# Kernel optimization log

Measured on AMD Instinct MI355X. Metric: run time of the kernel, lower is better.

## Reference

```python
import jax, jax.numpy as jnp
import numpy as np

EMBED = 2048
HEADS = 16
DFF = 4 * EMBED
EPS = 1e-5


def layernorm(x, g, b):
    mu = jnp.mean(x, axis=-1, keepdims=True)
    var = jnp.var(x, axis=-1, keepdims=True)
    return (x - mu) * jax.lax.rsqrt(var + EPS) * g + b


def setup_inputs() -> dict:
    key = jax.random.key(0)
    ks = jax.random.split(key, 16)
    s = 1.0 / np.sqrt(EMBED)
    sf = 1.0 / np.sqrt(DFF)
    return {
        "x": jax.random.normal(ks[0], (2, 2048, EMBED), jnp.float32),
        "Wq": jax.random.normal(ks[1], (EMBED, EMBED), jnp.float32) * s,
        "bq": jnp.zeros((EMBED,), jnp.float32),
        "Wk": jax.random.normal(ks[2], (EMBED, EMBED), jnp.float32) * s,
        "bk": jnp.zeros((EMBED,), jnp.float32),
        "Wv": jax.random.normal(ks[3], (EMBED, EMBED), jnp.float32) * s,
        "bv": jnp.zeros((EMBED,), jnp.float32),
        "Wo": jax.random.normal(ks[4], (EMBED, EMBED), jnp.float32) * s,
        "bo": jnp.zeros((EMBED,), jnp.float32),
        "g1": jnp.ones((EMBED,), jnp.float32),
        "b1": jnp.zeros((EMBED,), jnp.float32),
        "g2": jnp.ones((EMBED,), jnp.float32),
        "b2": jnp.zeros((EMBED,), jnp.float32),
        "W1": jax.random.normal(ks[5], (EMBED, DFF), jnp.float32) * s,
        "bf1": jnp.zeros((DFF,), jnp.float32),
        "W2": jax.random.normal(ks[6], (DFF, EMBED), jnp.float32) * sf,
        "bf2": jnp.zeros((EMBED,), jnp.float32),
    }


def reference(x, Wq, bq, Wk, bk, Wv, bv, Wo, bo, g1, b1, g2, b2, W1, bf1, W2, bf2):
    B, N, C = x.shape
    H = HEADS
    hd = C // H
    # QKV projections -> [B, H, N, hd]
    def split_heads(t):
        return t.reshape(B, N, H, hd).transpose(0, 2, 1, 3)
    q = split_heads(x @ Wq + bq)
    k = split_heads(x @ Wk + bk)
    v = split_heads(x @ Wv + bv)
    # scores [B, H, N, N]
    attn = jnp.einsum('bhqd,bhkd->bhqk', q, k) / np.sqrt(hd)
    attn = jax.nn.softmax(attn, axis=-1)
    out = jnp.einsum('bhqk,bhkd->bhqd', attn, v)
    out = out.transpose(0, 2, 1, 3).reshape(B, N, C)
    out = out @ Wo + bo
    h = layernorm(x + out, g1, b1)
    ff = jax.nn.gelu(h @ W1 + bf1, approximate=False) @ W2 + bf2
    return layernorm(h + ff, g2, b2)
```

## Files before the change

kernel.cpp:

```cpp
#include <hip/hip_runtime.h>
#include <math.h>

#define EMBED 2048
#define DFF   8192
#define TOK   4096
#define SEQ   2048
#define HEADS 16
#define HD    128
#define LDQ   6144

typedef __attribute__((ext_vector_type(8))) short short8;
typedef __attribute__((ext_vector_type(4))) float f32x4;

__device__ __forceinline__ unsigned short f2bf(float f) {
    unsigned int u = __float_as_uint(f);
    return (unsigned short)((u + 0x7FFFu + ((u >> 16) & 1u)) >> 16);
}
__device__ __forceinline__ float bf2f(unsigned short s) {
    return __uint_as_float(((unsigned int)s) << 16);
}

__device__ __forceinline__ void async16(const void* g, void* l) {
    __builtin_amdgcn_global_load_lds((const __attribute__((address_space(1))) void*)g,
                                     (__attribute__((address_space(3))) void*)l, 16, 0, 0);
}

__device__ __forceinline__ float gelu_fast(float v) {
    const float y = 1.5957691216057308f * (v + 0.044715f * v * v * v);
    return v / (1.0f + __expf(-y));
}

template<int MODE>
__global__ __launch_bounds__(256, 2)
void gemm_bf16(const unsigned short* __restrict__ A, const unsigned short* __restrict__ B,
               const float* __restrict__ bias, const void* __restrict__ resid,
               unsigned short* __restrict__ C, int M, int N, int K, int lda)
{
    __shared__ __align__(16) float smemf[8448];
    unsigned short* As = (unsigned short*)smemf;
    unsigned short* Bs = As + 8192;
    float* Cs = smemf;

    const int t = threadIdx.x;
    const int w = t >> 6, l = t & 63;
    const int quad = l >> 4, m16 = l & 15;
    const long bm = (long)blockIdx.y * 128, bn = (long)blockIdx.x * 128;
    const int wr = (w >> 1)*64, wc = (w & 1)*64;

    f32x4 acc[4][4] = {};

    const int srow = w*16 + (l >> 2);
    const int sslot = l & 3;
    const unsigned short* Ag = A + (size_t)bm*lda;
    const unsigned short* Bg = B + (size_t)bn*K;

#pragma unroll
    for (int u = 0; u < 2; ++u) {
        const int row = u*64 + srow;
        const int c = sslot ^ ((row >> 1) & 3);
        async16(Ag + (size_t)row*lda + c*8, &As[u*2048 + w*512]);
        async16(Bg + (size_t)row*K   + c*8, &Bs[u*2048 + w*512]);
    }

    const int iters = K >> 5;
    for (int it = 0; it < iters; ++it) {
        __syncthreads();
        if (it + 1 < iters) {
            const int k0 = (it + 1) << 5;
            const int bo = ((it + 1) & 1) * 4096;
#pragma unroll
            for (int u = 0; u < 2; ++u) {
                const int row = u*64 + srow;
                const int c = sslot ^ ((row >> 1) & 3);
                async16(Ag + (size_t)row*lda + k0 + c*8, &As[bo + u*2048 + w*512]);
                async16(Bg + (size_t)row*K   + k0 + c*8, &Bs[bo + u*2048 + w*512]);
            }
        }
        const int co = (it & 1) * 4096;
        short8 af[4], bf[4];
#pragma unroll
        for (int s = 0; s < 4; ++s) {
            const int ra = wr + s*16 + m16;
            const int sla = quad ^ ((ra >> 1) & 3);
            af[s] = *(const short8*)&As[co + ra*32 + sla*8];
            const int rb = wc + s*16 + m16;
            const int slb = quad ^ ((rb >> 1) & 3);
            bf[s] = *(const short8*)&Bs[co + rb*32 + slb*8];
        }
#pragma unroll
        for (int ms = 0; ms < 4; ++ms)
#pragma unroll
            for (int ns = 0; ns < 4; ++ns)
                acc[ms][ns] = __builtin_amdgcn_mfma_f32_16x16x32_bf16(af[ms], bf[ns], acc[ms][ns], 0, 0, 0);
    }

    const int ecol = (t & 15) * 8;
    float bias8[8];
#pragma unroll
    for (int i = 0; i < 8; ++i) bias8[i] = bias[bn + ecol + i];

#pragma unroll
    for (int pass = 0; pass < 2; ++pass) {
        __syncthreads();
        if ((w >> 1) == pass) {
#pragma unroll
            for (int ms = 0; ms < 4; ++ms)
#pragma unroll
                for (int ns = 0; ns < 4; ++ns)
#pragma unroll
                    for (int r = 0; r < 4; ++r)
                        Cs[(ms*16 + quad*4 + r)*132 + wc + ns*16 + m16] = acc[ms][ns][r];
        }
        __syncthreads();
#pragma unroll
        for (int j = 0; j < 4; ++j) {
            const int row = j*16 + (t >> 4);
            float v[8];
            *(f32x4*)&v[0] = *(const f32x4*)&Cs[row*132 + ecol];
            *(f32x4*)&v[4] = *(const f32x4*)&Cs[row*132 + ecol + 4];
            const long gr = bm + pass*64 + row;
            const long go = gr*N + bn + ecol;
            float r8[8];
            if (MODE == 1) {
                *(f32x4*)&r8[0] = *(const f32x4*)((const float*)resid + go);
                *(f32x4*)&r8[4] = *(const f32x4*)((const float*)resid + go + 4);
            }
            short8 rb16;
            if (MODE == 3) rb16 = *(const short8*)((const unsigned short*)resid + go);
            short8 o;
#pragma unroll
            for (int i = 0; i < 8; ++i) {
                float y = v[i] + bias8[i];
                if (MODE == 1) y += r8[i];
                if (MODE == 3) y += bf2f((unsigned short)rb16[i]);
                if (MODE == 2) y = gelu_fast(y);
                o[i] = (short)f2bf(y);
            }
            *(short8*)&C[go] = o;
        }
    }
}

__global__ __launch_bounds__(256, 2)
void attn_flash(unsigned short* __restrict__ qkv)
{
    __shared__ unsigned short Qs[64*128];
    __shared__ unsigned short Ks[64*128];
    __shared__ unsigned short Vt[128*72];
    __shared__ unsigned short Ps[4*16*72];

    const int t = threadIdx.x;
    const int w = t >> 6, l = t & 63;
    const int quad = l >> 4, m16 = l & 15;

    const int qt = blockIdx.x & 31;
    const int bh = blockIdx.x >> 5;
    const int b = bh >> 4, h = bh & 15;

    const long rowq = (long)b*SEQ + qt*64;
    const int qc = h*HD;
    const int kc = EMBED + h*HD;
    const int vc = 2*EMBED + h*HD;

    {
        const int rbase = w*4 + (l >> 4);
        const int slot = l & 15;
#pragma unroll
        for (int u = 0; u < 4; ++u) {
            const int row = u*16 + rbase;
            const int c = slot ^ ((row >> 1) & 7);
            async16(qkv + (rowq + row)*LDQ + qc + c*8, Qs + u*2048 + w*512);
        }
    }
    __syncthreads();

    short8 af[4];
#pragma unroll
    for (int ks = 0; ks < 4; ++ks) {
        const int row = w*16 + m16;
        const int sl = (4*ks + quad) ^ ((row >> 1) & 7);
        af[ks] = *(const short8*)&Qs[row*128 + sl*8];
    }

    f32x4 O[8] = {};
    float mrun[4] = {-1e30f,-1e30f,-1e30f,-1e30f};
    float lrun[4] = {0.f,0.f,0.f,0.f};
    unsigned short* Pw = Ps + w*16*72;

    for (int kt = 0; kt < SEQ/64; ++kt) {
        const long rowkv = (long)b*SEQ + kt*64;
        __syncthreads();
        {
            const int rbase = w*4 + (l >> 4);
            const int slot = l & 15;
#pragma unroll
            for (int u = 0; u < 4; ++u) {
                const int row = u*16 + rbase;
                const int c = slot ^ ((row >> 1) & 7);
                async16(qkv + (rowkv + row)*LDQ + kc + c*8, &Ks[u*2048 + w*512]);
            }
        }
        {
            const int slot = t & 15;
#pragma unroll
            for (int u = 0; u < 2; ++u) {
                const int rp = u*16 + (t >> 4);
                const short8 va = *(const short8*)(qkv + (rowkv + 2*rp    )*LDQ + vc + slot*8);
                const short8 vb = *(const short8*)(qkv + (rowkv + 2*rp + 1)*LDQ + vc + slot*8);
#pragma unroll
                for (int i = 0; i < 8; ++i) {
                    const int d = slot*8 + i;
                    const int col = (2*rp) ^ (((d >> 5) & 3) << 3);
                    unsigned int pv = (unsigned int)(unsigned short)va[i] |
                                      ((unsigned int)(unsigned short)vb[i] << 16);
                    *(unsigned int*)&Vt[d*72 + col] = pv;
                }
            }
        }
        __syncthreads();

        f32x4 S[4];
#pragma unroll
        for (int ns = 0; ns < 4; ++ns) {
            f32x4 a = {0.f,0.f,0.f,0.f};
            const int row = ns*16 + m16;
            const int swr = (row >> 1) & 7;
#pragma unroll
            for (int ks = 0; ks < 4; ++ks) {
                const int sl = (4*ks + quad) ^ swr;
                const short8 bfr = *(const short8*)&Ks[row*128 + sl*8];
                a = __builtin_amdgcn_mfma_f32_16x16x32_bf16(af[ks], bfr, a, 0, 0, 0);
            }
#pragma unroll
            for (int r = 0; r < 4; ++r) a[r] *= 0.08838834764831845f;
            S[ns] = a;
        }

        float al[4], rs[4];
#pragma unroll
        for (int r = 0; r < 4; ++r) {
            float tm = fmaxf(fmaxf(S[0][r], S[1][r]), fmaxf(S[2][r], S[3][r]));
            tm = fmaxf(tm, __shfl_xor(tm, 1));
            tm = fmaxf(tm, __shfl_xor(tm, 2));
            tm = fmaxf(tm, __shfl_xor(tm, 4));
            tm = fmaxf(tm, __shfl_xor(tm, 8));
            const float mn = fmaxf(mrun[r], tm);
            al[r] = __expf(mrun[r] - mn);
            mrun[r] = mn;
            rs[r] = 0.f;
        }
#pragma unroll
        for (int ns = 0; ns < 4; ++ns)
#pragma unroll
            for (int r = 0; r < 4; ++r) {
                const float p = __expf(S[ns][r] - mrun[r]);
                rs[r] += p;
                Pw[(quad*4 + r)*72 + ns*16 + m16] = f2bf(p);
            }
#pragma unroll
        for (int r = 0; r < 4; ++r) {
            rs[r] += __shfl_xor(rs[r], 1);
            rs[r] += __shfl_xor(rs[r], 2);
            rs[r] += __shfl_xor(rs[r], 4);
            rs[r] += __shfl_xor(rs[r], 8);
            lrun[r] = lrun[r]*al[r] + rs[r];
        }
#pragma unroll
        for (int i = 0; i < 8; ++i)
#pragma unroll
            for (int r = 0; r < 4; ++r) O[i][r] *= al[r];

#pragma unroll
        for (int ks2 = 0; ks2 < 2; ++ks2) {
            const short8 ap = *(const short8*)&Pw[m16*72 + ks2*32 + quad*8];
#pragma unroll
            for (int ds = 0; ds < 8; ++ds) {
                const int d = ds*16 + m16;
                const int jcol = (ks2*32 + quad*8) ^ (((d >> 5) & 3) << 3);
                const short8 bv = *(const short8*)&Vt[d*72 + jcol];
                O[ds] = __builtin_amdgcn_mfma_f32_16x16x32_bf16(ap, bv, O[ds], 0, 0, 0);
            }
        }
    }

    float inv[4];
#pragma unroll
    for (int r = 0; r < 4; ++r) inv[r] = 1.0f / lrun[r];
#pragma unroll
    for (int ds = 0; ds < 8; ++ds)
#pragma unroll
        for (int r = 0; r < 4; ++r) {
            const long row = rowq + w*16 + quad*4 + r;
            qkv[row*LDQ + qc + ds*16 + m16] = f2bf(O[ds][r] * inv[r]);
        }
}

template<int OUTF32>
__global__ __launch_bounds__(256)
void ln_bf16(const unsigned short* __restrict__ X, const float* __restrict__ g,
             const float* __restrict__ be, void* __restrict__ Y)
{
    __shared__ float r1[256], r2[256];
    const int t = threadIdx.x;
    const long row = blockIdx.x;
    const unsigned short* x = X + row*EMBED;
    float v[8];
    const short8 xv = *(const short8*)(x + t*8);
    float s = 0.f, s2 = 0.f;
#pragma unroll
    for (int i = 0; i < 8; ++i) {
        v[i] = bf2f((unsigned short)xv[i]);
        s += v[i]; s2 += v[i]*v[i];
    }
    r1[t] = s; r2[t] = s2;
    __syncthreads();
    for (int k = 128; k > 0; k >>= 1) {
        if (t < k) { r1[t] += r1[t+k]; r2[t] += r2[t+k]; }
        __syncthreads();
    }
    const float mu = r1[0] * (1.0f/EMBED);
    const float var = r2[0] * (1.0f/EMBED) - mu*mu;
    const float rstd = rsqrtf(var + 1e-5f);
    if (OUTF32) {
        float* y = (float*)Y + row*EMBED + t*8;
#pragma unroll
        for (int i = 0; i < 8; ++i) y[i] = (v[i]-mu)*rstd*g[t*8+i] + be[t*8+i];
    } else {
        unsigned short* y = (unsigned short*)Y + row*EMBED;
        short8 o;
#pragma unroll
        for (int i = 0; i < 8; ++i) o[i] = (short)f2bf((v[i]-mu)*rstd*g[t*8+i] + be[t*8+i]);
        *(short8*)(y + t*8) = o;
    }
}

__global__ __launch_bounds__(256)
void cvt_transpose(const float* __restrict__ W, unsigned short* __restrict__ Wt, int K, int N)
{
    __shared__ unsigned short T[32][33];
    const int t = threadIdx.x;
    const long n0 = (long)blockIdx.x*32, k0 = (long)blockIdx.y*32;
    {
        const int r = t >> 3, c = (t & 7)*4;
        const float4 vv = *(const float4*)&W[(k0 + r)*N + n0 + c];
        T[r][c+0] = f2bf(vv.x); T[r][c+1] = f2bf(vv.y);
        T[r][c+2] = f2bf(vv.z); T[r][c+3] = f2bf(vv.w);
    }
    __syncthreads();
    const int rn = t >> 3, kk = (t & 7)*4;
    unsigned int p0 = (unsigned int)T[kk+0][rn] | ((unsigned int)T[kk+1][rn] << 16);
    unsigned int p1 = (unsigned int)T[kk+2][rn] | ((unsigned int)T[kk+3][rn] << 16);
    unsigned int* dst = (unsigned int*)&Wt[(n0 + rn)*K + k0 + kk];
    dst[0] = p0; dst[1] = p1;
}

__global__ __launch_bounds__(256)
void cvt_f32_bf16(const float* __restrict__ X, unsigned short* __restrict__ Y, long n)
{
    const long i = ((long)blockIdx.x*256 + threadIdx.x)*8;
    if (i >= n) return;
    const float4 a = *(const float4*)&X[i];
    const float4 b = *(const float4*)&X[i+4];
    short8 o;
    o[0]=(short)f2bf(a.x); o[1]=(short)f2bf(a.y); o[2]=(short)f2bf(a.z); o[3]=(short)f2bf(a.w);
    o[4]=(short)f2bf(b.x); o[5]=(short)f2bf(b.y); o[6]=(short)f2bf(b.z); o[7]=(short)f2bf(b.w);
    *(short8*)&Y[i] = o;
}

__global__ __launch_bounds__(256)
void concat_bias(const float* __restrict__ bq, const float* __restrict__ bk,
                 const float* __restrict__ bv, float* __restrict__ out)
{
    const int i = blockIdx.x*256 + threadIdx.x;
    if (i < 2048) out[i] = bq[i];
    else if (i < 4096) out[i] = bk[i-2048];
    else if (i < 6144) out[i] = bv[i-4096];
}

extern "C" void kernel_launch(void* const* d_in, const int* in_sizes, int n_in,
                              void* d_out, int out_size, void* d_ws, size_t ws_size,
                              hipStream_t stream)
{
    const float* x   = (const float*)d_in[0];
    const float* Wq  = (const float*)d_in[1];
    const float* bq  = (const float*)d_in[2];
    const float* Wk  = (const float*)d_in[3];
    const float* bk  = (const float*)d_in[4];
    const float* Wv  = (const float*)d_in[5];
    const float* bv  = (const float*)d_in[6];
    const float* Wo  = (const float*)d_in[7];
    const float* bo  = (const float*)d_in[8];
    const float* g1  = (const float*)d_in[9];
    const float* b1  = (const float*)d_in[10];
    const float* g2v = (const float*)d_in[11];
    const float* b2v = (const float*)d_in[12];
    const float* W1  = (const float*)d_in[13];
    const float* bf1 = (const float*)d_in[14];
    const float* W2  = (const float*)d_in[15];
    const float* bf2 = (const float*)d_in[16];
    float* out = (float*)d_out;

    char* ws = (char*)d_ws;
    unsigned short* Wqkvt = (unsigned short*)(ws + 0);
    unsigned short* Wot   = (unsigned short*)(ws + 25165824);
    unsigned short* W1t   = (unsigned short*)(ws + 33554432);
    unsigned short* W2t   = (unsigned short*)(ws + 67108864);
    float*          bqkv  = (float*)         (ws + 100663296);
    char* arenaA = ws + 100687872;
    unsigned short* xb   = (unsigned short*)(arenaA);
    unsigned short* qkv  = (unsigned short*)(arenaA + 16777216);
    unsigned short* res1 = (unsigned short*)(arenaA);
    unsigned short* ff   = (unsigned short*)(arenaA);
    unsigned short* hb   = (unsigned short*)(ws + 167796736);
    unsigned short* res2 = (unsigned short*)(ws + 0);

    const dim3 blk(256);

    cvt_transpose<<<dim3(64,64),  blk, 0, stream>>>(Wq, Wqkvt,             2048, 2048);
    cvt_transpose<<<dim3(64,64),  blk, 0, stream>>>(Wk, Wqkvt + 2048*2048, 2048, 2048);
    cvt_transpose<<<dim3(64,64),  blk, 0, stream>>>(Wv, Wqkvt + 2*2048*2048, 2048, 2048);
    cvt_transpose<<<dim3(64,64),  blk, 0, stream>>>(Wo, Wot, 2048, 2048);
    cvt_transpose<<<dim3(256,64), blk, 0, stream>>>(W1, W1t, 2048, 8192);
    cvt_transpose<<<dim3(64,256), blk, 0, stream>>>(W2, W2t, 8192, 2048);
    concat_bias<<<dim3(24), blk, 0, stream>>>(bq, bk, bv, bqkv);
    cvt_f32_bf16<<<dim3(4096), blk, 0, stream>>>(x, xb, (long)TOK*EMBED);

    gemm_bf16<0><<<dim3(48,32), blk, 0, stream>>>(xb, Wqkvt, bqkv, nullptr, qkv, TOK, 6144, 2048, 2048);
    attn_flash<<<dim3(1024), blk, 0, stream>>>(qkv);
    gemm_bf16<1><<<dim3(16,32), blk, 0, stream>>>(qkv, Wot, bo, x, res1, TOK, 2048, 2048, 6144);
    ln_bf16<0><<<dim3(4096), blk, 0, stream>>>(res1, g1, b1, hb);
    gemm_bf16<2><<<dim3(64,32), blk, 0, stream>>>(hb, W1t, bf1, nullptr, ff, TOK, 8192, 2048, 2048);
    gemm_bf16<3><<<dim3(16,32), blk, 0, stream>>>(ff, W2t, bf2, hb, res2, TOK, 2048, 8192, 8192);
    ln_bf16<1><<<dim3(4096), blk, 0, stream>>>(res2, g2v, b2v, out);
}
```

Baseline: 951.4 us.

## Pre-transpose V in a separate kernel and async-load it in flash attention

A new kernel writes V transposed per batch-head into workspace. The attention kernel can then bring V tiles into LDS with swizzled async global-to-LDS copies, replacing the per-iteration register transpose with scalar LDS stores. Q staging now shares the V buffer and the P padding changes, which shrinks LDS so launch bounds can target three blocks per SM. The cost is an extra kernel launch and a round trip of V through global memory, plus an added barrier at the end of each iteration.

```diff
diff --git a/kernel.cpp b/kernel.cpp
--- a/kernel.cpp
+++ b/kernel.cpp
@@ -10,6 +10,7 @@
 #define LDQ   6144
 
 typedef __attribute__((ext_vector_type(8))) short short8;
+typedef __attribute__((ext_vector_type(4))) short short4v;
 typedef __attribute__((ext_vector_type(4))) float f32x4;
 
 __device__ __forceinline__ unsigned short f2bf(float f) {
@@ -141,13 +142,35 @@
     }
 }
 
-__global__ __launch_bounds__(256, 2)
-void attn_flash(unsigned short* __restrict__ qkv)
-{
-    __shared__ unsigned short Qs[64*128];
+__global__ __launch_bounds__(256)
+void transpose_v(const unsigned short* __restrict__ qkv, unsigned short* __restrict__ VT)
+{
+    __shared__ unsigned short T[32*34];
+    const int t = threadIdx.x;
+    const int bh = blockIdx.z, b = bh >> 4, h = bh & 15;
+    const long j0 = (long)blockIdx.x*32;
+    const int d0 = blockIdx.y*32;
+    {
+        const int r = t >> 3, c4 = (t & 7)*4;
+        const short4v v = *(const short4v*)&qkv[((long)b*SEQ + j0 + r)*LDQ + 2*EMBED + h*HD + d0 + c4];
+#pragma unroll
+        for (int i = 0; i < 4; ++i) T[r*34 + c4 + i] = (unsigned short)v[i];
+    }
+    __syncthreads();
+    const int rn = t >> 3, kk = (t & 7)*4;
+    short4v o;
+#pragma unroll
+    for (int i = 0; i < 4; ++i) o[i] = (short)T[(kk + i)*34 + rn];
+    *(short4v*)&VT[((long)bh*HD + d0 + rn)*SEQ + j0 + kk] = o;
+}
+
+__global__ __launch_bounds__(256, 3)
+void attn_flash(unsigned short* __restrict__ qkv, const unsigned short* __restrict__ VT)
+{
     __shared__ unsigned short Ks[64*128];
-    __shared__ unsigned short Vt[128*72];
-    __shared__ unsigned short Ps[4*16*72];
+    __shared__ unsigned short Vt[128*64];
+    __shared__ unsigned short Ps[4*16*76];
+    unsigned short* Qs = Vt;
 
     const int t = threadIdx.x;
     const int w = t >> 6, l = t & 63;
@@ -160,17 +183,15 @@
     const long rowq = (long)b*SEQ + qt*64;
     const int qc = h*HD;
     const int kc = EMBED + h*HD;
-    const int vc = 2*EMBED + h*HD;
-
-    {
-        const int rbase = w*4 + (l >> 4);
-        const int slot = l & 15;
-#pragma unroll
-        for (int u = 0; u < 4; ++u) {
-            const int row = u*16 + rbase;
-            const int c = slot ^ ((row >> 1) & 7);
-            async16(qkv + (rowq + row)*LDQ + qc + c*8, Qs + u*2048 + w*512);
-        }
+
+    const int rbase = w*4 + (l >> 4);
+    const int slot16 = l & 15;
+
+#pragma unroll
+    for (int u = 0; u < 4; ++u) {
+        const int row = u*16 + rbase;
+        const int c = slot16 ^ ((row >> 1) & 7);
+        async16(qkv + (rowq + row)*LDQ + qc + c*8, Qs + u*2048 + w*512);
     }
     __syncthreads();
 
@@ -181,41 +202,26 @@
         const int sl = (4*ks + quad) ^ ((row >> 1) & 7);
         af[ks] = *(const short8*)&Qs[row*128 + sl*8];
     }
+    __syncthreads();
 
     f32x4 O[8] = {};
     float mrun[4] = {-1e30f,-1e30f,-1e30f,-1e30f};
     float lrun[4] = {0.f,0.f,0.f,0.f};
-    unsigned short* Pw = Ps + w*16*72;
+    unsigned short* Pw = Ps + w*16*76;
 
     for (int kt = 0; kt < SEQ/64; ++kt) {
         const long rowkv = (long)b*SEQ + kt*64;
-        __syncthreads();
-        {
-            const int rbase = w*4 + (l >> 4);
-            const int slot = l & 15;
-#pragma unroll
-            for (int u = 0; u < 4; ++u) {
-                const int row = u*16 + rbase;
-                const int c = slot ^ ((row >> 1) & 7);
-                async16(qkv + (rowkv + row)*LDQ + kc + c*8, &Ks[u*2048 + w*512]);
-            }
-        }
-        {
-            const int slot = t & 15;
-#pragma unroll
-            for (int u = 0; u < 2; ++u) {
-                const int rp = u*16 + (t >> 4);
-                const short8 va = *(const short8*)(qkv + (rowkv + 2*rp    )*LDQ + vc + slot*8);
-                const short8 vb = *(const short8*)(qkv + (rowkv + 2*rp + 1)*LDQ + vc + slot*8);
-#pragma unroll
-                for (int i = 0; i < 8; ++i) {
-                    const int d = slot*8 + i;
-                    const int col = (2*rp) ^ (((d >> 5) & 3) << 3);
-                    unsigned int pv = (unsigned int)(unsigned short)va[i] |
-                                      ((unsigned int)(unsigned short)vb[i] << 16);
-                    *(unsigned int*)&Vt[d*72 + col] = pv;
-                }
-            }
+#pragma unroll
+        for (int u = 0; u < 4; ++u) {
+            const int row = u*16 + rbase;
+            const int c = slot16 ^ ((row >> 1) & 7);
+            async16(qkv + (rowkv + row)*LDQ + kc + c*8, &Ks[u*2048 + w*512]);
+        }
+#pragma unroll
+        for (int u = 0; u < 4; ++u) {
+            const int vd = (w*4 + u)*8 + (l >> 3);
+            const int c  = (l & 7) ^ (vd & 7);
+            async16(VT + ((long)bh*HD + vd)*SEQ + kt*64 + c*8, &Vt[(w*4 + u)*512]);
         }
         __syncthreads();
 
@@ -255,7 +261,7 @@
             for (int r = 0; r < 4; ++r) {
                 const float p = __expf(S[ns][r] - mrun[r]);
                 rs[r] += p;
-                Pw[(quad*4 + r)*72 + ns*16 + m16] = f2bf(p);
+                Pw[(quad*4 + r)*76 + ns*16 + m16] = f2bf(p);
             }
 #pragma unroll
         for (int r = 0; r < 4; ++r) {
@@ -272,15 +278,16 @@
 
 #pragma unroll
         for (int ks2 = 0; ks2 < 2; ++ks2) {
-            const short8 ap = *(const short8*)&Pw[m16*72 + ks2*32 + quad*8];
+            const short8 ap = *(const short8*)&Pw[m16*76 + ks2*32 + quad*8];
 #pragma unroll
             for (int ds = 0; ds < 8; ++ds) {
                 const int d = ds*16 + m16;
-                const int jcol = (ks2*32 + quad*8) ^ (((d >> 5) & 3) << 3);
-                const short8 bv = *(const short8*)&Vt[d*72 + jcol];
+                const int csw = (ks2*4 + quad) ^ (d & 7);
+                const short8 bv = *(const short8*)&Vt[d*64 + csw*8];
                 O[ds] = __builtin_amdgcn_mfma_f32_16x16x32_bf16(ap, bv, O[ds], 0, 0, 0);
             }
         }
+        __syncthreads();
     }
 
     float inv[4];
@@ -409,6 +416,7 @@
     char* arenaA = ws + 100687872;
     unsigned short* xb   = (unsigned short*)(arenaA);
     unsigned short* qkv  = (unsigned short*)(arenaA + 16777216);
+    unsigned short* VT   = (unsigned short*)(ws + 0);
     unsigned short* res1 = (unsigned short*)(arenaA);
     unsigned short* ff   = (unsigned short*)(arenaA);
     unsigned short* hb   = (unsigned short*)(ws + 167796736);
@@ -426,7 +434,8 @@
     cvt_f32_bf16<<<dim3(4096), blk, 0, stream>>>(x, xb, (long)TOK*EMBED);
 
     gemm_bf16<0><<<dim3(48,32), blk, 0, stream>>>(xb, Wqkvt, bqkv, nullptr, qkv, TOK, 6144, 2048, 2048);
-    attn_flash<<<dim3(1024), blk, 0, stream>>>(qkv);
+    transpose_v<<<dim3(64,4,32), blk, 0, stream>>>(qkv, VT);
+    attn_flash<<<dim3(1024), blk, 0, stream>>>(qkv, VT);
     gemm_bf16<1><<<dim3(16,32), blk, 0, stream>>>(qkv, Wot, bo, x, res1, TOK, 2048, 2048, 6144);
     ln_bf16<0><<<dim3(4096), blk, 0, stream>>>(res1, g1, b1, hb);
     gemm_bf16<2><<<dim3(64,32), blk, 0, stream>>>(hb, W1t, bf1, nullptr, ff, TOK, 8192, 2048, 2048);
```

New measurement: 987.2 us. 3.8% more time.
